# Kernel optimization log

Measured on AMD Instinct MI355X. Metric: run time of the kernel, lower is better.

## Reference

```python
import jax, jax.numpy as jnp
import numpy as np

D = 1024          # d_model
H = 16            # num_attention_heads
HD = D // H       # head_dim
WIN = 512         # attention_window (total)
W = WIN // 2      # one-sided window
S = 4096          # seq_len
B = 2             # batch
NEG = jnp.finfo(jnp.float32).min


def setup_inputs() -> dict:
    key = jax.random.key(0)
    ks = jax.random.split(key, 9)
    sc = 0.02
    return {
        "query": jax.random.normal(ks[0], (S, B, D), dtype=jnp.float32),
        "Wq": jax.random.normal(ks[1], (D, D), dtype=jnp.float32) * sc,
        "bq": jnp.zeros((D,), dtype=jnp.float32),
        "Wk": jax.random.normal(ks[2], (D, D), dtype=jnp.float32) * sc,
        "bk": jnp.zeros((D,), dtype=jnp.float32),
        "Wv": jax.random.normal(ks[3], (D, D), dtype=jnp.float32) * sc,
        "bv": jnp.zeros((D,), dtype=jnp.float32),
        "Wo": jax.random.normal(ks[4], (D, D), dtype=jnp.float32) * sc,
        "bo": jnp.zeros((D,), dtype=jnp.float32),
    }


def _heads(x):  # [B,S,D] -> [B,H,S,HD]
    b, s, _ = x.shape
    return x.reshape(b, s, H, HD).transpose(0, 2, 1, 3)


def reference(query, Wq, bq, Wk, bk, Wv, bv, Wo, bo):
    s, b, d = query.shape
    x = query.transpose(1, 0, 2)                       # [B,S,D]
    q = _heads(x @ Wq + bq) / jnp.sqrt(jnp.float32(HD))  # [B,H,S,HD]
    k = _heads(x @ Wk + bk)
    v = _heads(x @ Wv + bv)

    nc = s // W                                        # number of chunks
    # pad keys/values with one window of zeros on each side of seq axis
    kp = jnp.pad(k, ((0, 0), (0, 0), (W, W), (0, 0)))  # [B,H,S+2W,HD]
    vp = jnp.pad(v, ((0, 0), (0, 0), (W, W), (0, 0)))
    idx = jnp.arange(nc)[:, None] * W + jnp.arange(3 * W)[None, :]  # [nc,3W]
    kc = kp[:, :, idx]                                 # [B,H,nc,3W,HD]
    vc = vp[:, :, idx]
    qc = q.reshape(b, H, nc, W, HD)                    # [B,H,nc,W,HD]

    scores = jnp.einsum("bhcrd,bhckd->bhcrk", qc, kc)  # [B,H,nc,W,3W]

    r = jnp.arange(W)[:, None]                         # query offset in chunk
    kk = jnp.arange(3 * W)[None, :]
    band = (kk >= r) & (kk <= r + 2 * W)               # |kpos-qpos| <= W
    kpos = jnp.arange(nc)[:, None, None] * W + kk[None] - W   # [nc,1,3W] global key pos
    mask = band[None] & (kpos >= 0) & (kpos < s)       # [nc,W,3W]

    scores = jnp.where(mask[None, None], scores, NEG)
    probs = jax.nn.softmax(scores, axis=-1)
    out = jnp.einsum("bhcrk,bhckd->bhcrd", probs, vc)  # [B,H,nc,W,HD]
    out = out.reshape(b, H, s, HD).transpose(0, 2, 1, 3).reshape(b, s, d)
    out = out.transpose(1, 0, 2)                       # [S,B,D]
    return out @ Wo + bo
```

## Files before the change

### kernel.cpp

```cpp
#include <hip/hip_runtime.h>
#include <hip/hip_bf16.h>

#define SEQ 4096
#define BATCH 2
#define DMODEL 1024
#define NH 16
#define HDIM 64
#define NEGM (-1.0e30f)
#define NT 16

typedef __attribute__((ext_vector_type(8))) short bf16x8;
typedef __attribute__((ext_vector_type(8))) unsigned short us8;
typedef __attribute__((ext_vector_type(4))) unsigned short us4;
typedef __attribute__((ext_vector_type(4))) float f32x4;

__device__ __forceinline__ unsigned short f2bf(float f) {
    union { float f; unsigned u; } v; v.f = f;
    unsigned u = v.u;
    return (unsigned short)((u + 0x7fffu + ((u >> 16) & 1u)) >> 16);
}

#define GL16(g, l)                                                              \
    __builtin_amdgcn_global_load_lds(                                           \
        (const __attribute__((address_space(1))) unsigned int*)(g),             \
        (__attribute__((address_space(3))) unsigned int*)(l), 16, 0, 0)

__global__ __launch_bounds__(256) void transpose_w(const float* __restrict__ W,
                                                   unsigned short* __restrict__ Wt,
                                                   float scale) {
    __shared__ float tile[64][65];
    const int n0 = blockIdx.x * 64, k0 = blockIdx.y * 64;
    const int tx = threadIdx.x;
    for (int dy = threadIdx.y; dy < 64; dy += 4)
        tile[dy][tx] = W[(size_t)(k0 + dy) * DMODEL + n0 + tx];
    __syncthreads();
    for (int dy = threadIdx.y; dy < 64; dy += 4)
        Wt[(size_t)(n0 + dy) * DMODEL + k0 + tx] = f2bf(tile[tx][dy] * scale);
}

__global__ __launch_bounds__(256) void build_bcat(const float* __restrict__ bq,
                                                  const float* __restrict__ bk,
                                                  const float* __restrict__ bv,
                                                  float* __restrict__ bcat) {
    int i = blockIdx.x * 256 + threadIdx.x;
    float v;
    if (i < 1024) v = bq[i] * 0.125f;
    else if (i < 2048) v = bk[i - 1024];
    else v = bv[i - 2048];
    bcat[i] = v;
}

__global__ __launch_bounds__(256) void convert_x(const float* __restrict__ q,
                                                 unsigned short* __restrict__ xb) {
    int t = blockIdx.x * 256 + threadIdx.x;
    int d4 = (t & 255) * 4;
    int row = t >> 8;
    int b = row >> 12, s = row & (SEQ - 1);
    float4 v = *(const float4*)(q + ((size_t)s * BATCH + b) * DMODEL + d4);
    us4 o;
    o[0] = f2bf(v.x); o[1] = f2bf(v.y); o[2] = f2bf(v.z); o[3] = f2bf(v.w);
    *(us4*)(xb + (size_t)row * DMODEL + d4) = o;
}

template <int MODE>
__device__ __forceinline__ void gemm_epilogue(f32x4 (&acc)[4][4], int m0, int n0,
                                              int wm, int wn, int lr, int lg,
                                              const float* __restrict__ bias,
                                              unsigned short* __restrict__ qb,
                                              unsigned short* __restrict__ kb,
                                              unsigned short* __restrict__ vtb,
                                              float* __restrict__ out) {
#pragma unroll
    for (int fn = 0; fn < 4; ++fn) {
        const int col = n0 + wn * 64 + fn * 16 + lr;
        const float bval = bias[col];
#pragma unroll
        for (int fm = 0; fm < 4; ++fm) {
            const int row0 = m0 + wm * 64 + fm * 16 + lg * 4;
            if (MODE == 0) {
                const int proj = col >> 10;
                const int ch = col & 1023;
                const int h = ch >> 6, hd = ch & 63;
                if (proj == 2) {
                    const int b = row0 >> 12, s = row0 & (SEQ - 1);
                    us4 o;
#pragma unroll
                    for (int r = 0; r < 4; ++r) o[r] = f2bf(acc[fm][fn][r] + bval);
                    *(us4*)(vtb + ((size_t)(b * NH + h) * HDIM + hd) * SEQ + s) = o;
                } else {
                    unsigned short* dst = (proj == 0) ? qb : kb;
#pragma unroll
                    for (int r = 0; r < 4; ++r) {
                        const int row = row0 + r;
                        const int b = row >> 12, s = row & (SEQ - 1);
                        dst[((size_t)(b * NH + h) * SEQ + s) * HDIM + hd] = f2bf(acc[fm][fn][r] + bval);
                    }
                }
            } else {
#pragma unroll
                for (int r = 0; r < 4; ++r) {
                    const int row = row0 + r;
                    const int b = row >> 12, s = row & (SEQ - 1);
                    out[((size_t)s * BATCH + b) * DMODEL + col] = acc[fm][fn][r] + bval;
                }
            }
        }
    }
}

template <int MODE, int NBX>
__global__ __launch_bounds__(512, 4) void gemm256sb(const unsigned short* __restrict__ A,
                                                    const unsigned short* __restrict__ Bt,
                                                    const float* __restrict__ bias,
                                                    unsigned short* __restrict__ qb,
                                                    unsigned short* __restrict__ kb,
                                                    unsigned short* __restrict__ vtb,
                                                    float* __restrict__ out) {
    __shared__ __align__(16) unsigned short lds[24576];
    const int tid = threadIdx.x;
    const int lane = tid & 63, wid = tid >> 6;
    const int lr = lane & 15, lg = lane >> 4;
    const int wm = wid >> 1, wn = wid & 1;
    const int cpx = (int)gridDim.x >> 3;
    const int orig = ((int)blockIdx.x & 7) * cpx + ((int)blockIdx.x >> 3);
    const int m0 = (orig / NBX) * 256;
    const int n0 = (orig % NBX) * 128;

    const int srow = wid * 8 + (lane >> 3);
    const int scol = ((lane & 7) ^ (lane >> 3)) << 3;

    f32x4 acc[4][4];
#pragma unroll
    for (int m = 0; m < 4; ++m)
#pragma unroll
        for (int n = 0; n < 4; ++n) {
            f32x4 z = {0.f, 0.f, 0.f, 0.f};
            acc[m][n] = z;
        }

    const unsigned short* gA = A + (size_t)(m0 + srow) * DMODEL + scol;
    const unsigned short* gB = Bt + (size_t)(n0 + srow) * DMODEL + scol;
    const int swz = (lr & 7) << 3;

    for (int t = 0; t < NT; ++t) {
        {
            const unsigned short* ga_ = gA + t * 64;
            unsigned short* la_ = &lds[wid * 512];
#pragma unroll
            for (int r_ = 0; r_ < 4; ++r_)
                GL16(ga_ + (size_t)r_ * 64 * DMODEL, la_ + r_ * 4096);
            const unsigned short* gb_ = gB + t * 64;
            unsigned short* lb_ = &lds[16384 + wid * 512];
#pragma unroll
            for (int r_ = 0; r_ < 2; ++r_)
                GL16(gb_ + (size_t)r_ * 64 * DMODEL, lb_ + r_ * 4096);
        }
        asm volatile("s_waitcnt vmcnt(0)" ::: "memory");
        __builtin_amdgcn_s_barrier();
        asm volatile("" ::: "memory");
#pragma unroll
        for (int ks = 0; ks < 2; ++ks) {
            const int kc = (ks * 32 + lg * 8) ^ swz;
            bf16x8 af[4], bfr[4];
#pragma unroll
            for (int fm = 0; fm < 4; ++fm)
                af[fm] = *(const bf16x8*)&lds[(wm * 64 + fm * 16 + lr) * 64 + kc];
#pragma unroll
            for (int fn = 0; fn < 4; ++fn)
                bfr[fn] = *(const bf16x8*)&lds[16384 + (wn * 64 + fn * 16 + lr) * 64 + kc];
            __builtin_amdgcn_s_setprio(1);
#pragma unroll
            for (int fm = 0; fm < 4; ++fm)
#pragma unroll
                for (int fn = 0; fn < 4; ++fn)
                    acc[fm][fn] = __builtin_amdgcn_mfma_f32_16x16x32_bf16(af[fm], bfr[fn], acc[fm][fn], 0, 0, 0);
            __builtin_amdgcn_s_setprio(0);
        }
        __builtin_amdgcn_sched_barrier(0);
        asm volatile("s_waitcnt lgkmcnt(0)" ::: "memory");
        __builtin_amdgcn_s_barrier();
        asm volatile("" ::: "memory");
    }

    gemm_epilogue<MODE>(acc, m0, n0, wm, wn, lr, lg, bias, qb, kb, vtb, out);
}

template <int MODE, int NBX>
__global__ __launch_bounds__(512) void gemm256(const unsigned short* __restrict__ A,
                                               const unsigned short* __restrict__ Bt,
                                               const float* __restrict__ bias,
                                               unsigned short* __restrict__ qb,
                                               unsigned short* __restrict__ kb,
                                               unsigned short* __restrict__ vtb,
                                               float* __restrict__ out) {
    __shared__ __align__(16) unsigned short lds[73728];
    const int tid = threadIdx.x;
    const int lane = tid & 63, wid = tid >> 6;
    const int lr = lane & 15, lg = lane >> 4;
    const int wm = wid >> 1, wn = wid & 1;
    const int cpx = (int)gridDim.x >> 3;
    const int orig = ((int)blockIdx.x & 7) * cpx + ((int)blockIdx.x >> 3);
    const int m0 = (orig / NBX) * 256;
    const int n0 = (orig % NBX) * 128;

    const int srow = wid * 8 + (lane >> 3);
    const int scol = ((lane & 7) ^ (lane >> 3)) << 3;

    f32x4 acc[4][4];
#pragma unroll
    for (int m = 0; m < 4; ++m)
#pragma unroll
        for (int n = 0; n < 4; ++n) {
            f32x4 z = {0.f, 0.f, 0.f, 0.f};
            acc[m][n] = z;
        }

    const unsigned short* gA = A + (size_t)(m0 + srow) * DMODEL + scol;
    const unsigned short* gB = Bt + (size_t)(n0 + srow) * DMODEL + scol;

#define STAGE_A(kt, bsel)                                                        \
    do {                                                                         \
        const unsigned short* ga_ = gA + (kt) * 64;                              \
        unsigned short* la_ = &lds[(bsel) * 24576 + wid * 512];                  \
        _Pragma("unroll")                                                        \
        for (int r_ = 0; r_ < 4; ++r_)                                           \
            GL16(ga_ + (size_t)r_ * 64 * DMODEL, la_ + r_ * 4096);               \
    } while (0)
#define STAGE_B(kt, bsel)                                                        \
    do {                                                                         \
        const unsigned short* gb_ = gB + (kt) * 64;                              \
        unsigned short* lb_ = &lds[(bsel) * 24576 + 16384 + wid * 512];          \
        _Pragma("unroll")                                                        \
        for (int r_ = 0; r_ < 2; ++r_)                                           \
            GL16(gb_ + (size_t)r_ * 64 * DMODEL, lb_ + r_ * 4096);               \
    } while (0)

    STAGE_A(0, 0); STAGE_B(0, 0);
    STAGE_A(1, 1); STAGE_B(1, 1);
    asm volatile("s_waitcnt vmcnt(6)" ::: "memory");
    __builtin_amdgcn_s_barrier();
    asm volatile("" ::: "memory");

    const int swz = (lr & 7) << 3;
    int bs = 0;
    for (int t = 0; t < NT; ++t) {
        const int b2 = bs >= 1 ? bs - 1 : bs + 2;
        if (t + 2 < NT) { STAGE_A(t + 2, b2); STAGE_B(t + 2, b2); }
        const unsigned short* Ab = &lds[bs * 24576];
        const unsigned short* Bb = Ab + 16384;
#pragma unroll
        for (int ks = 0; ks < 2; ++ks) {
            const int kc = (ks * 32 + lg * 8) ^ swz;
            bf16x8 af[4], bfr[4];
#pragma unroll
            for (int fm = 0; fm < 4; ++fm)
                af[fm] = *(const bf16x8*)&Ab[(wm * 64 + fm * 16 + lr) * 64 + kc];
#pragma unroll
            for (int fn = 0; fn < 4; ++fn)
                bfr[fn] = *(const bf16x8*)&Bb[(wn * 64 + fn * 16 + lr) * 64 + kc];
            __builtin_amdgcn_s_setprio(1);
#pragma unroll
            for (int fm = 0; fm < 4; ++fm)
#pragma unroll
                for (int fn = 0; fn < 4; ++fn)
                    acc[fm][fn] = __builtin_amdgcn_mfma_f32_16x16x32_bf16(af[fm], bfr[fn], acc[fm][fn], 0, 0, 0);
            __builtin_amdgcn_s_setprio(0);
        }
        __builtin_amdgcn_sched_barrier(0);
        asm volatile("s_waitcnt lgkmcnt(0)" ::: "memory");
        if (t + 2 < NT)
            asm volatile("s_waitcnt vmcnt(6)" ::: "memory");
        else
            asm volatile("s_waitcnt vmcnt(0)" ::: "memory");
        __builtin_amdgcn_s_barrier();
        asm volatile("" ::: "memory");
        bs = bs < 2 ? bs + 1 : 0;
    }
#undef STAGE_A
#undef STAGE_B

    gemm_epilogue<MODE>(acc, m0, n0, wm, wn, lr, lg, bias, qb, kb, vtb, out);
}

__global__ __launch_bounds__(512) void attn_kernel(const unsigned short* __restrict__ qb,
                                                   const unsigned short* __restrict__ kb,
                                                   const unsigned short* __restrict__ vtb,
                                                   unsigned short* __restrict__ ao) {
    __shared__ __align__(16) unsigned short Ks[64][72];
    __shared__ __align__(16) unsigned short Vs[64][72];
    __shared__ __align__(16) unsigned short Ps[8][16][72];
    const int tid = threadIdx.x;
    const int lane = tid & 63, wid = tid >> 6;
    const int lr = lane & 15, lg = lane >> 4;
    const int blk = ((int)blockIdx.x & 7) * 128 + ((int)blockIdx.x >> 3);
    const int qc = blk & 31, h = (blk >> 5) & 15, b = blk >> 9;
    const int q0 = qc * 128;
    const unsigned short* Qh = qb + (size_t)(b * NH + h) * SEQ * HDIM;
    const unsigned short* Kh = kb + (size_t)(b * NH + h) * SEQ * HDIM;
    const unsigned short* Vh = vtb + (size_t)(b * NH + h) * HDIM * SEQ;
    const int qw = q0 + wid * 16;

    bf16x8 qf0 = *(const bf16x8*)(Qh + (size_t)(qw + lr) * HDIM + lg * 8);
    bf16x8 qf1 = *(const bf16x8*)(Qh + (size_t)(qw + lr) * HDIM + 32 + lg * 8);

    f32x4 oacc[4];
    float lsum[4];
#pragma unroll
    for (int n = 0; n < 4; ++n) {
        f32x4 z = {0.f, 0.f, 0.f, 0.f};
        oacc[n] = z;
    }
#pragma unroll
    for (int r = 0; r < 4; ++r) lsum[r] = 0.f;

    int lo = q0 - 256; if (lo < 0) lo = 0;
    int hi = q0 + 384; if (hi > SEQ) hi = SEQ;

    const int srow = tid >> 3, sseg = (tid & 7) * 8;

    us8 kpre = *(const us8*)(Kh + (size_t)(lo + srow) * HDIM + sseg);
    us8 vpre = *(const us8*)(Vh + (size_t)srow * SEQ + lo + sseg);

    for (int kt = lo; kt < hi; kt += 64) {
        __syncthreads();
        *(us8*)&Ks[srow][sseg] = kpre;
        *(us8*)&Vs[srow][sseg] = vpre;
        if (kt + 64 < hi) {
            kpre = *(const us8*)(Kh + (size_t)(kt + 64 + srow) * HDIM + sseg);
            vpre = *(const us8*)(Vh + (size_t)srow * SEQ + kt + 64 + sseg);
        }
        __builtin_amdgcn_sched_barrier(0);
        __syncthreads();

        f32x4 sf[4];
        __builtin_amdgcn_s_setprio(1);
#pragma unroll
        for (int n = 0; n < 4; ++n) {
            bf16x8 kf0 = *(const bf16x8*)&Ks[n * 16 + lr][lg * 8];
            bf16x8 kf1 = *(const bf16x8*)&Ks[n * 16 + lr][32 + lg * 8];
            f32x4 z = {0.f, 0.f, 0.f, 0.f};
            sf[n] = __builtin_amdgcn_mfma_f32_16x16x32_bf16(qf0, kf0, z, 0, 0, 0);
            sf[n] = __builtin_amdgcn_mfma_f32_16x16x32_bf16(qf1, kf1, sf[n], 0, 0, 0);
        }
        __builtin_amdgcn_s_setprio(0);
        const bool full = (kt >= qw - 241) && (kt + 63 <= qw + 256);
        if (!full) {
#pragma unroll
            for (int r = 0; r < 4; ++r) {
                const int qpos = qw + lg * 4 + r;
#pragma unroll
                for (int n = 0; n < 4; ++n) {
                    const int kpos = kt + n * 16 + lr;
                    if (kpos < qpos - 256 || kpos > qpos + 256) sf[n][r] = NEGM;
                }
            }
        }
#pragma unroll
        for (int n = 0; n < 4; ++n)
#pragma unroll
            for (int r = 0; r < 4; ++r) {
                const float p = __expf(sf[n][r]);
                lsum[r] += p;
                Ps[wid][lg * 4 + r][n * 16 + lr] = f2bf(p);
            }

        asm volatile("s_waitcnt lgkmcnt(0)" ::: "memory");
        __builtin_amdgcn_s_setprio(1);
#pragma unroll
        for (int ks = 0; ks < 2; ++ks) {
            bf16x8 pf = *(const bf16x8*)&Ps[wid][lr][ks * 32 + lg * 8];
#pragma unroll
            for (int n = 0; n < 4; ++n) {
                bf16x8 vf = *(const bf16x8*)&Vs[n * 16 + lr][ks * 32 + lg * 8];
                oacc[n] = __builtin_amdgcn_mfma_f32_16x16x32_bf16(pf, vf, oacc[n], 0, 0, 0);
            }
        }
        __builtin_amdgcn_s_setprio(0);
    }

#pragma unroll
    for (int d = 1; d < 16; d <<= 1)
#pragma unroll
        for (int r = 0; r < 4; ++r) lsum[r] += __shfl_xor(lsum[r], d, 64);

#pragma unroll
    for (int n = 0; n < 4; ++n)
#pragma unroll
        for (int r = 0; r < 4; ++r) {
            const int row = qw + lg * 4 + r;
            const float o = oacc[n][r] / lsum[r];
            ao[((size_t)b * SEQ + row) * DMODEL + h * HDIM + n * 16 + lr] = f2bf(o);
        }
}

extern "C" void kernel_launch(void* const* d_in, const int* in_sizes, int n_in,
                              void* d_out, int out_size, void* d_ws, size_t ws_size,
                              hipStream_t stream) {
    (void)in_sizes; (void)n_in; (void)out_size; (void)ws_size;
    const float* query = (const float*)d_in[0];
    const float* Wq = (const float*)d_in[1];
    const float* bq = (const float*)d_in[2];
    const float* Wk = (const float*)d_in[3];
    const float* bk = (const float*)d_in[4];
    const float* Wv = (const float*)d_in[5];
    const float* bv = (const float*)d_in[6];
    const float* Wo = (const float*)d_in[7];
    const float* bo = (const float*)d_in[8];
    float* out = (float*)d_out;

    char* ws = (char*)d_ws;
    unsigned short* xb   = (unsigned short*)ws;
    unsigned short* wcat = (unsigned short*)(ws + (16ull << 20));
    unsigned short* wot  = (unsigned short*)(ws + (22ull << 20));
    float*          bcat = (float*)(ws + (24ull << 20));
    unsigned short* qb   = (unsigned short*)(ws + (25ull << 20));
    unsigned short* kb   = (unsigned short*)(ws + (41ull << 20));
    unsigned short* vtb  = (unsigned short*)(ws + (57ull << 20));
    unsigned short* ao   = xb;

    transpose_w<<<dim3(16, 16), dim3(64, 4), 0, stream>>>(Wq, wcat, 0.125f);
    transpose_w<<<dim3(16, 16), dim3(64, 4), 0, stream>>>(Wk, wcat + 1024 * 1024, 1.0f);
    transpose_w<<<dim3(16, 16), dim3(64, 4), 0, stream>>>(Wv, wcat + 2 * 1024 * 1024, 1.0f);
    transpose_w<<<dim3(16, 16), dim3(64, 4), 0, stream>>>(Wo, wot, 1.0f);
    build_bcat<<<12, 256, 0, stream>>>(bq, bk, bv, bcat);
    convert_x<<<8192, 256, 0, stream>>>(query, xb);

    gemm256sb<0, 24><<<768, 512, 0, stream>>>(xb, wcat, bcat, qb, kb, vtb, nullptr);
    attn_kernel<<<1024, 512, 0, stream>>>(qb, kb, vtb, ao);
    gemm256<1, 8><<<256, 512, 0, stream>>>(ao, wot, bo, nullptr, nullptr, nullptr, out);
}
```

Baseline: 173.9 us.

## Replace QKV GEMM with 256x192 double-buffered tile kernel

The fused QKV projection GEMM moves from a single-buffered 256x128 tile (768 blocks, 4 per CU) to a 256x192 tile with two LDS buffers (512 blocks). The next K-slice is prefetched while the current one is computed, and each wave now computes an 8x3 grid of MFMA fragments instead of 4x4. This aims to cut load stalls and raise operand reuse per LDS read. In exchange it uses more LDS (about 112KB) and more accumulator registers, which lowers occupancy, and it still waits on vmcnt(0) every iteration. The output-projection GEMM is only specialised, with no change in behaviour.

```diff
diff --git a/kernel.cpp b/kernel.cpp
--- a/kernel.cpp
+++ b/kernel.cpp
@@ -62,137 +62,130 @@
     *(us4*)(xb + (size_t)row * DMODEL + d4) = o;
 }
 
-template <int MODE>
-__device__ __forceinline__ void gemm_epilogue(f32x4 (&acc)[4][4], int m0, int n0,
-                                              int wm, int wn, int lr, int lg,
-                                              const float* __restrict__ bias,
-                                              unsigned short* __restrict__ qb,
-                                              unsigned short* __restrict__ kb,
-                                              unsigned short* __restrict__ vtb,
-                                              float* __restrict__ out) {
-#pragma unroll
-    for (int fn = 0; fn < 4; ++fn) {
-        const int col = n0 + wn * 64 + fn * 16 + lr;
-        const float bval = bias[col];
-#pragma unroll
-        for (int fm = 0; fm < 4; ++fm) {
-            const int row0 = m0 + wm * 64 + fm * 16 + lg * 4;
-            if (MODE == 0) {
-                const int proj = col >> 10;
-                const int ch = col & 1023;
-                const int h = ch >> 6, hd = ch & 63;
-                if (proj == 2) {
-                    const int b = row0 >> 12, s = row0 & (SEQ - 1);
-                    us4 o;
-#pragma unroll
-                    for (int r = 0; r < 4; ++r) o[r] = f2bf(acc[fm][fn][r] + bval);
-                    *(us4*)(vtb + ((size_t)(b * NH + h) * HDIM + hd) * SEQ + s) = o;
-                } else {
-                    unsigned short* dst = (proj == 0) ? qb : kb;
-#pragma unroll
-                    for (int r = 0; r < 4; ++r) {
-                        const int row = row0 + r;
-                        const int b = row >> 12, s = row & (SEQ - 1);
-                        dst[((size_t)(b * NH + h) * SEQ + s) * HDIM + hd] = f2bf(acc[fm][fn][r] + bval);
-                    }
-                }
-            } else {
-#pragma unroll
-                for (int r = 0; r < 4; ++r) {
-                    const int row = row0 + r;
-                    const int b = row >> 12, s = row & (SEQ - 1);
-                    out[((size_t)s * BATCH + b) * DMODEL + col] = acc[fm][fn][r] + bval;
-                }
-            }
-        }
-    }
-}
-
-template <int MODE, int NBX>
-__global__ __launch_bounds__(512, 4) void gemm256sb(const unsigned short* __restrict__ A,
-                                                    const unsigned short* __restrict__ Bt,
-                                                    const float* __restrict__ bias,
-                                                    unsigned short* __restrict__ qb,
-                                                    unsigned short* __restrict__ kb,
-                                                    unsigned short* __restrict__ vtb,
-                                                    float* __restrict__ out) {
-    __shared__ __align__(16) unsigned short lds[24576];
-    const int tid = threadIdx.x;
-    const int lane = tid & 63, wid = tid >> 6;
-    const int lr = lane & 15, lg = lane >> 4;
-    const int wm = wid >> 1, wn = wid & 1;
-    const int cpx = (int)gridDim.x >> 3;
-    const int orig = ((int)blockIdx.x & 7) * cpx + ((int)blockIdx.x >> 3);
-    const int m0 = (orig / NBX) * 256;
-    const int n0 = (orig % NBX) * 128;
-
-    const int srow = wid * 8 + (lane >> 3);
-    const int scol = ((lane & 7) ^ (lane >> 3)) << 3;
-
-    f32x4 acc[4][4];
-#pragma unroll
-    for (int m = 0; m < 4; ++m)
-#pragma unroll
-        for (int n = 0; n < 4; ++n) {
-            f32x4 z = {0.f, 0.f, 0.f, 0.f};
-            acc[m][n] = z;
-        }
-
-    const unsigned short* gA = A + (size_t)(m0 + srow) * DMODEL + scol;
-    const unsigned short* gB = Bt + (size_t)(n0 + srow) * DMODEL + scol;
-    const int swz = (lr & 7) << 3;
-
-    for (int t = 0; t < NT; ++t) {
-        {
-            const unsigned short* ga_ = gA + t * 64;
-            unsigned short* la_ = &lds[wid * 512];
-#pragma unroll
-            for (int r_ = 0; r_ < 4; ++r_)
-                GL16(ga_ + (size_t)r_ * 64 * DMODEL, la_ + r_ * 4096);
-            const unsigned short* gb_ = gB + t * 64;
-            unsigned short* lb_ = &lds[16384 + wid * 512];
-#pragma unroll
-            for (int r_ = 0; r_ < 2; ++r_)
-                GL16(gb_ + (size_t)r_ * 64 * DMODEL, lb_ + r_ * 4096);
-        }
-        asm volatile("s_waitcnt vmcnt(0)" ::: "memory");
-        __builtin_amdgcn_s_barrier();
-        asm volatile("" ::: "memory");
-#pragma unroll
-        for (int ks = 0; ks < 2; ++ks) {
-            const int kc = (ks * 32 + lg * 8) ^ swz;
-            bf16x8 af[4], bfr[4];
-#pragma unroll
-            for (int fm = 0; fm < 4; ++fm)
-                af[fm] = *(const bf16x8*)&lds[(wm * 64 + fm * 16 + lr) * 64 + kc];
-#pragma unroll
-            for (int fn = 0; fn < 4; ++fn)
-                bfr[fn] = *(const bf16x8*)&lds[16384 + (wn * 64 + fn * 16 + lr) * 64 + kc];
-            __builtin_amdgcn_s_setprio(1);
-#pragma unroll
-            for (int fm = 0; fm < 4; ++fm)
-#pragma unroll
-                for (int fn = 0; fn < 4; ++fn)
-                    acc[fm][fn] = __builtin_amdgcn_mfma_f32_16x16x32_bf16(af[fm], bfr[fn], acc[fm][fn], 0, 0, 0);
-            __builtin_amdgcn_s_setprio(0);
-        }
-        __builtin_amdgcn_sched_barrier(0);
-        asm volatile("s_waitcnt lgkmcnt(0)" ::: "memory");
-        __builtin_amdgcn_s_barrier();
-        asm volatile("" ::: "memory");
-    }
-
-    gemm_epilogue<MODE>(acc, m0, n0, wm, wn, lr, lg, bias, qb, kb, vtb, out);
-}
-
-template <int MODE, int NBX>
-__global__ __launch_bounds__(512) void gemm256(const unsigned short* __restrict__ A,
+__device__ __forceinline__ void store_qkv(float v0, float v1, float v2, float v3,
+                                          int row0, int col, float bval,
+                                          unsigned short* __restrict__ qb,
+                                          unsigned short* __restrict__ kb,
+                                          unsigned short* __restrict__ vtb) {
+    const int proj = col >> 10;
+    const int ch = col & 1023;
+    const int h = ch >> 6, hd = ch & 63;
+    float vv[4] = {v0, v1, v2, v3};
+    if (proj == 2) {
+        const int b = row0 >> 12, s = row0 & (SEQ - 1);
+        us4 o;
+#pragma unroll
+        for (int r = 0; r < 4; ++r) o[r] = f2bf(vv[r] + bval);
+        *(us4*)(vtb + ((size_t)(b * NH + h) * HDIM + hd) * SEQ + s) = o;
+    } else {
+        unsigned short* dst = (proj == 0) ? qb : kb;
+#pragma unroll
+        for (int r = 0; r < 4; ++r) {
+            const int row = row0 + r;
+            const int b = row >> 12, s = row & (SEQ - 1);
+            dst[((size_t)(b * NH + h) * SEQ + s) * HDIM + hd] = f2bf(vv[r] + bval);
+        }
+    }
+}
+
+__global__ __launch_bounds__(512) void gemm192(const unsigned short* __restrict__ A,
                                                const unsigned short* __restrict__ Bt,
                                                const float* __restrict__ bias,
                                                unsigned short* __restrict__ qb,
                                                unsigned short* __restrict__ kb,
-                                               unsigned short* __restrict__ vtb,
-                                               float* __restrict__ out) {
+                                               unsigned short* __restrict__ vtb) {
+    __shared__ __align__(16) unsigned short lds[57344];
+    const int tid = threadIdx.x;
+    const int lane = tid & 63, wid = tid >> 6;
+    const int lr = lane & 15, lg = lane >> 4;
+    const int wm = wid >> 2, wn = wid & 3;
+    const int cpx = (int)gridDim.x >> 3;
+    const int orig = ((int)blockIdx.x & 7) * cpx + ((int)blockIdx.x >> 3);
+    const int m0 = (orig >> 4) * 256;
+    const int n0 = (orig & 15) * 192;
+
+    const int srow = wid * 8 + (lane >> 3);
+    const int scol = ((lane & 7) ^ (lane >> 3)) << 3;
+
+    f32x4 acc[8][3];
+#pragma unroll
+    for (int m = 0; m < 8; ++m)
+#pragma unroll
+        for (int n = 0; n < 3; ++n) {
+            f32x4 z = {0.f, 0.f, 0.f, 0.f};
+            acc[m][n] = z;
+        }
+
+    const unsigned short* gA = A + (size_t)(m0 + srow) * DMODEL + scol;
+    const unsigned short* gB = Bt + (size_t)(n0 + srow) * DMODEL + scol;
+
+#define STAGE192(kt, bsel)                                                       \
+    do {                                                                         \
+        const unsigned short* ga_ = gA + (kt) * 64;                              \
+        unsigned short* la_ = &lds[(bsel) * 28672 + wid * 512];                  \
+        _Pragma("unroll")                                                        \
+        for (int r_ = 0; r_ < 4; ++r_)                                           \
+            GL16(ga_ + (size_t)r_ * 64 * DMODEL, la_ + r_ * 4096);               \
+        const unsigned short* gb_ = gB + (kt) * 64;                              \
+        unsigned short* lb_ = &lds[(bsel) * 28672 + 16384 + wid * 512];          \
+        _Pragma("unroll")                                                        \
+        for (int r_ = 0; r_ < 3; ++r_)                                           \
+            GL16(gb_ + (size_t)r_ * 64 * DMODEL, lb_ + r_ * 4096);               \
+    } while (0)
+
+    STAGE192(0, 0);
+    asm volatile("s_waitcnt vmcnt(0)" ::: "memory");
+    __builtin_amdgcn_s_barrier();
+    asm volatile("" ::: "memory");
+
+    const int swz = (lr & 7) << 3;
+    for (int t = 0; t < NT; ++t) {
+        if (t + 1 < NT) STAGE192(t + 1, (t + 1) & 1);
+        const unsigned short* Ab = &lds[(t & 1) * 28672];
+        const unsigned short* Bb = Ab + 16384;
+#pragma unroll
+        for (int ks = 0; ks < 2; ++ks) {
+            const int kc = (ks * 32 + lg * 8) ^ swz;
+            bf16x8 af[8], bfr[3];
+#pragma unroll
+            for (int fm = 0; fm < 8; ++fm)
+                af[fm] = *(const bf16x8*)&Ab[(wm * 128 + fm * 16 + lr) * 64 + kc];
+#pragma unroll
+            for (int fn = 0; fn < 3; ++fn)
+                bfr[fn] = *(const bf16x8*)&Bb[(wn * 48 + fn * 16 + lr) * 64 + kc];
+            __builtin_amdgcn_s_setprio(1);
+#pragma unroll
+            for (int fm = 0; fm < 8; ++fm)
+#pragma unroll
+                for (int fn = 0; fn < 3; ++fn)
+                    acc[fm][fn] = __builtin_amdgcn_mfma_f32_16x16x32_bf16(af[fm], bfr[fn], acc[fm][fn], 0, 0, 0);
+            __builtin_amdgcn_s_setprio(0);
+        }
+        __builtin_amdgcn_sched_barrier(0);
+        asm volatile("s_waitcnt lgkmcnt(0)" ::: "memory");
+        asm volatile("s_waitcnt vmcnt(0)" ::: "memory");
+        __builtin_amdgcn_s_barrier();
+        asm volatile("" ::: "memory");
+    }
+#undef STAGE192
+
+#pragma unroll
+    for (int fn = 0; fn < 3; ++fn) {
+        const int col = n0 + wn * 48 + fn * 16 + lr;
+        const float bval = bias[col];
+#pragma unroll
+        for (int fm = 0; fm < 8; ++fm) {
+            const int row0 = m0 + wm * 128 + fm * 16 + lg * 4;
+            store_qkv(acc[fm][fn][0], acc[fm][fn][1], acc[fm][fn][2], acc[fm][fn][3],
+                      row0, col, bval, qb, kb, vtb);
+        }
+    }
+}
+
+__global__ __launch_bounds__(512) void gemm256o(const unsigned short* __restrict__ A,
+                                                const unsigned short* __restrict__ Bt,
+                                                const float* __restrict__ bias,
+                                                float* __restrict__ out) {
     __shared__ __align__(16) unsigned short lds[73728];
     const int tid = threadIdx.x;
     const int lane = tid & 63, wid = tid >> 6;
@@ -200,8 +193,8 @@
     const int wm = wid >> 1, wn = wid & 1;
     const int cpx = (int)gridDim.x >> 3;
     const int orig = ((int)blockIdx.x & 7) * cpx + ((int)blockIdx.x >> 3);
-    const int m0 = (orig / NBX) * 256;
-    const int n0 = (orig % NBX) * 128;
+    const int m0 = (orig >> 3) * 256;
+    const int n0 = (orig & 7) * 128;
 
     const int srow = wid * 8 + (lane >> 3);
     const int scol = ((lane & 7) ^ (lane >> 3)) << 3;
@@ -279,7 +272,21 @@
 #undef STAGE_A
 #undef STAGE_B
 
-    gemm_epilogue<MODE>(acc, m0, n0, wm, wn, lr, lg, bias, qb, kb, vtb, out);
+#pragma unroll
+    for (int fn = 0; fn < 4; ++fn) {
+        const int col = n0 + wn * 64 + fn * 16 + lr;
+        const float bval = bias[col];
+#pragma unroll
+        for (int fm = 0; fm < 4; ++fm) {
+            const int row0 = m0 + wm * 64 + fm * 16 + lg * 4;
+#pragma unroll
+            for (int r = 0; r < 4; ++r) {
+                const int row = row0 + r;
+                const int b = row >> 12, s = row & (SEQ - 1);
+                out[((size_t)s * BATCH + b) * DMODEL + col] = acc[fm][fn][r] + bval;
+            }
+        }
+    }
 }
 
 __global__ __launch_bounds__(512) void attn_kernel(const unsigned short* __restrict__ qb,
@@ -425,7 +432,7 @@
     build_bcat<<<12, 256, 0, stream>>>(bq, bk, bv, bcat);
     convert_x<<<8192, 256, 0, stream>>>(query, xb);
 
-    gemm256sb<0, 24><<<768, 512, 0, stream>>>(xb, wcat, bcat, qb, kb, vtb, nullptr);
+    gemm192<<<512, 512, 0, stream>>>(xb, wcat, bcat, qb, kb, vtb);
     attn_kernel<<<1024, 512, 0, stream>>>(qb, kb, vtb, ao);
-    gemm256<1, 8><<<256, 512, 0, stream>>>(ao, wot, bo, nullptr, nullptr, nullptr, out);
-}
+    gemm256o<<<256, 512, 0, stream>>>(ao, wot, bo, out);
+}
```

New measurement: 169.1 us. 1.03x faster.
